# Optimization experiments

Measured on AMD Instinct MI355X. Metric: run time of the kernel, lower is better.

The kernel has to match this reference:

```python
import jax, jax.numpy as jnp
import numpy as np

H = 256          # hidden_channels
NP, NJ, NC = 8192, 8192, 4096  # person / job_posting / company node counts
EA, EW, EP = 262144, 131072, 131072  # edge counts per relation


def _gcn(x_src, W, b, edge_index, num_src, num_dst):
    """Bipartite GCNConv: h = x_src @ W; out[dst] = sum_e norm_e * h[src_e] + b,
    norm = deg_out(src)^-1/2 * deg_in(dst)^-1/2 (symmetric GCN normalization)."""
    h = x_src @ W                                # [num_src, H]
    row, col = edge_index[0], edge_index[1]
    ones = jnp.ones(row.shape[0], dtype=h.dtype)
    deg_src = jax.ops.segment_sum(ones, row, num_segments=num_src)
    deg_dst = jax.ops.segment_sum(ones, col, num_segments=num_dst)
    dis_src = jnp.where(deg_src > 0, jax.lax.rsqrt(jnp.maximum(deg_src, 1e-12)), 0.0)
    dis_dst = jnp.where(deg_dst > 0, jax.lax.rsqrt(jnp.maximum(deg_dst, 1e-12)), 0.0)
    norm = dis_src[row] * dis_dst[col]           # [E]
    out = jax.ops.segment_sum(h[row] * norm[:, None], col, num_segments=num_dst)
    return out + b


def setup_inputs() -> dict:
    key = jax.random.key(0)
    ks = jax.random.split(key, 12)
    s = 1.0 / np.sqrt(H)
    return {
        "x_person":  jax.random.normal(ks[0], (NP, H), jnp.float32),
        "x_job":     jax.random.normal(ks[1], (NJ, H), jnp.float32),
        "x_company": jax.random.normal(ks[2], (NC, H), jnp.float32),
        "ei_applied": jax.random.randint(ks[3], (2, EA), 0, 8192, jnp.int64 if jax.config.read('jax_enable_x64') else jnp.int32),
        "ei_worked":  jax.random.randint(ks[4], (2, EW), 0, 4096, jnp.int64 if jax.config.read('jax_enable_x64') else jnp.int32),
        "ei_posted":  jax.random.randint(ks[5], (2, EP), 0, 4096, jnp.int64 if jax.config.read('jax_enable_x64') else jnp.int32),
        "W_aj": jax.random.normal(ks[6], (H, H), jnp.float32) * s,
        "b_aj": jnp.zeros((H,), jnp.float32),
        "W_wa": jax.random.normal(ks[7], (H, H), jnp.float32) * s,
        "b_wa": jnp.zeros((H,), jnp.float32),
        "W_pb": jax.random.normal(ks[8], (H, H), jnp.float32) * s,
        "b_pb": jnp.zeros((H,), jnp.float32),
    }


def reference(x_person, x_job, x_company, ei_applied, ei_worked, ei_posted,
              W_aj, b_aj, W_wa, b_wa, W_pb, b_pb):
    Np, Nj, Nc = x_person.shape[0], x_job.shape[0], x_company.shape[0]
    # HeteroConv with aggr='sum': each dst type sums messages over its edge types
    job_emb = _gcn(x_person, W_aj, b_aj, ei_applied, Np, Nj)
    comp_emb = (_gcn(x_person, W_wa, b_wa, ei_worked, Np, Nc)
                + _gcn(x_job, W_pb, b_pb, ei_posted, Nj, Nc))  # computed but unused downstream
    del comp_emb
    person_emb = x_person  # 'person' is never a dst type; features pass through
    scores = jax.nn.sigmoid(person_emb @ job_emb.T)  # [Np, Nj]
    return scores
```

## Files before the change

### kernel.cpp

```cpp
#include <hip/hip_runtime.h>
#include <hip/hip_bf16.h>

#define HCH 256
#define NPN 8192
#define NJN 8192
#define EAE 262144
#define CAP 96

typedef _Float16 f16x8 __attribute__((ext_vector_type(8)));
typedef _Float16 f16x4 __attribute__((ext_vector_type(4)));
typedef float f32x4 __attribute__((ext_vector_type(4)));

typedef __attribute__((address_space(1))) void glb_void;
typedef __attribute__((address_space(3))) void lds_void;

#define WS_CUR   0
#define WS_DEG   32768
#define WS_CSR2  65536
#define WS_XH    3211264
#define WS_ZH    7405568
#define WS_GH    11599872
#define WS_WHT   15794176

__global__ void k_edgeconv(const int* __restrict__ row, const int* __restrict__ col,
                           int* __restrict__ deg_src, int* __restrict__ cur,
                           int* __restrict__ csr2, const float* __restrict__ W,
                           _Float16* __restrict__ WhT, const float* __restrict__ x,
                           _Float16* __restrict__ Xh) {
    int bid = blockIdx.x, t = threadIdx.x;
    if (bid < 1024) {
        int e = bid * 256 + t;
        int r = row[e], c = col[e];
        atomicAdd(&deg_src[r], 1);
        int p = atomicAdd(&cur[c], 1);
        if (p < CAP) csr2[c * CAP + p] = r;
    } else if (bid < 1280) {
        int idx = (bid - 1024) * 256 + t;
        int n = idx >> 8, k = idx & 255;
        WhT[idx] = (_Float16)W[k * HCH + n];
    } else {
        int i = ((bid - 1280) * 256 + t) * 4;
        float4 v = *(const float4*)(x + i);
        f16x4 h;
        h[0] = (_Float16)v.x; h[1] = (_Float16)v.y;
        h[2] = (_Float16)v.z; h[3] = (_Float16)v.w;
        *(f16x4*)(Xh + i) = h;
    }
}

__global__ __launch_bounds__(64)
void k_agg(const _Float16* __restrict__ Xh, const int* __restrict__ csr2,
           const int* __restrict__ cur, const int* __restrict__ deg_src,
           _Float16* __restrict__ Zh) {
    int j = blockIdx.x;
    int t = threadIdx.x;
    int degt = cur[j];
    int deg = degt > CAP ? CAP : degt;

    __shared__ int   sidx[CAP];
    __shared__ float sw[CAP];
    for (int b = t; b < deg; b += 64) {
        int s = csr2[j * CAP + b];
        sidx[b] = s;
        sw[b] = rsqrtf((float)deg_src[s]);
    }
    __syncthreads();

    float a0 = 0.f, a1 = 0.f, a2 = 0.f, a3 = 0.f;
    const _Float16* xb = Xh + t * 4;
    int e = 0;
    for (; e + 4 <= deg; e += 4) {
        int s0 = sidx[e], s1 = sidx[e + 1], s2 = sidx[e + 2], s3 = sidx[e + 3];
        float w0 = sw[e], w1 = sw[e + 1], w2 = sw[e + 2], w3 = sw[e + 3];
        f16x4 v0 = *(const f16x4*)(xb + (size_t)s0 * HCH);
        f16x4 v1 = *(const f16x4*)(xb + (size_t)s1 * HCH);
        f16x4 v2 = *(const f16x4*)(xb + (size_t)s2 * HCH);
        f16x4 v3 = *(const f16x4*)(xb + (size_t)s3 * HCH);
        a0 += w0 * (float)v0[0] + w1 * (float)v1[0] + w2 * (float)v2[0] + w3 * (float)v3[0];
        a1 += w0 * (float)v0[1] + w1 * (float)v1[1] + w2 * (float)v2[1] + w3 * (float)v3[1];
        a2 += w0 * (float)v0[2] + w1 * (float)v1[2] + w2 * (float)v2[2] + w3 * (float)v3[2];
        a3 += w0 * (float)v0[3] + w1 * (float)v1[3] + w2 * (float)v2[3] + w3 * (float)v3[3];
    }
    for (; e < deg; e++) {
        int s0 = sidx[e];
        float w0 = sw[e];
        f16x4 v0 = *(const f16x4*)(xb + (size_t)s0 * HCH);
        a0 += w0 * (float)v0[0]; a1 += w0 * (float)v0[1];
        a2 += w0 * (float)v0[2]; a3 += w0 * (float)v0[3];
    }
    f16x4 out;
    if (degt > 0) {
        float dd = rsqrtf((float)degt);
        out[0] = (_Float16)(a0 * dd); out[1] = (_Float16)(a1 * dd);
        out[2] = (_Float16)(a2 * dd); out[3] = (_Float16)(a3 * dd);
    } else {
        out[0] = out[1] = out[2] = out[3] = (_Float16)0.f;
    }
    *(f16x4*)(Zh + (size_t)j * HCH + t * 4) = out;
}

template <int TM, int TN>
__global__ __launch_bounds__(256, 2)
void k_gemm(const _Float16* __restrict__ A, const _Float16* __restrict__ Bt,
            const float* __restrict__ bias, _Float16* __restrict__ Cout, int Ncols) {
    constexpr int WM = TM / 2, WN = TN / 2;
    constexpr int MR = WM / 16, NR = WN / 16;
    constexpr int CHA = TM * 8 / 256;
    constexpr int CHB = TN * 8 / 256;
    constexpr int BOFF = TM * 128;

    __shared__ _Float16 sm[2][(TM + TN) * 64];

    int tid = threadIdx.x;
    int wid = tid >> 6, lane = tid & 63;

    int brow = blockIdx.y * TM;
    int bcol = blockIdx.x * TN;
    int wrow = (wid >> 1) * WM;
    int wcol = (wid & 1) * WN;

    f32x4 acc[MR][NR] = {};

    int lr = lane & 15;
    int kq = lane >> 4;

    auto stage = [&](int t, int b) {
        int k0 = t * 64;
#pragma unroll
        for (int i = 0; i < CHA; i++) {
            int wc0 = i * 256 + wid * 64;
            int c = wc0 + lane;
            int r = c >> 3, cc = c & 7;
            const char* ga = (const char*)A +
                (size_t)(brow + r) * (HCH * 2) + (size_t)(k0 + cc * 8) * 2;
            __builtin_amdgcn_global_load_lds(
                (glb_void*)ga, (lds_void*)((char*)sm[b] + wc0 * 16), 16, 0, 0);
        }
#pragma unroll
        for (int i = 0; i < CHB; i++) {
            int wc0 = i * 256 + wid * 64;
            int c = wc0 + lane;
            int r = c >> 3, cc = c & 7;
            const char* gb = (const char*)Bt +
                (size_t)(bcol + r) * (HCH * 2) + (size_t)(k0 + cc * 8) * 2;
            __builtin_amdgcn_global_load_lds(
                (glb_void*)gb, (lds_void*)((char*)sm[b] + BOFF + wc0 * 16), 16, 0, 0);
        }
    };

    stage(0, 0);
    __syncthreads();

    constexpr int NT = HCH / 64;
#pragma unroll
    for (int t = 0; t < NT; t++) {
        int cur = t & 1;
        if (t + 1 < NT) stage(t + 1, cur ^ 1);
        const char* base = (const char*)sm[cur];
#pragma unroll
        for (int kk = 0; kk < 64; kk += 32) {
            f16x8 af[MR], bfr[NR];
            int kbyte = (kk + kq * 8) * 2;
#pragma unroll
            for (int m = 0; m < MR; m++) {
                int r = wrow + m * 16 + lr;
                af[m] = *(const f16x8*)(base + r * 128 + kbyte);
            }
#pragma unroll
            for (int n = 0; n < NR; n++) {
                int r = wcol + n * 16 + lr;
                bfr[n] = *(const f16x8*)(base + BOFF + r * 128 + kbyte);
            }
#pragma unroll
            for (int m = 0; m < MR; m++)
#pragma unroll
                for (int n = 0; n < NR; n++)
                    acc[m][n] = __builtin_amdgcn_mfma_f32_16x16x32_f16(
                        af[m], bfr[n], acc[m][n], 0, 0, 0);
        }
        __syncthreads();
    }

    int rq = lane >> 4;
#pragma unroll
    for (int m = 0; m < MR; m++) {
#pragma unroll
        for (int n = 0; n < NR; n++) {
#pragma unroll
            for (int j = 0; j < 4; j++) {
                int gr = brow + wrow + m * 16 + rq * 4 + j;
                int gc = bcol + wcol + n * 16 + lr;
                float v = acc[m][n][j] + bias[gc];
                Cout[(size_t)gr * Ncols + gc] = (_Float16)v;
            }
        }
    }
}

#define G2_NW 32
__global__ __launch_bounds__(512, 1)
void k_gemm2(const _Float16* __restrict__ A, const _Float16* __restrict__ Bt,
             float* __restrict__ C) {
    __shared__ _Float16 smA[128 * HCH];
    __shared__ _Float16 smB[2][64 * HCH];
    __shared__ float    smC[128 * 64];

    int tid = threadIdx.x;
    int wid = tid >> 6, lane = tid & 63;
    int lr = lane & 15, kq = lane >> 4;

    int id = blockIdx.x;
    int xcd = id & 7, slot = id >> 3;
    int cg = xcd >> 1;
    int strip = slot + (xcd & 1) * 32;
    int brow = strip * 128;
    int bcol0 = cg * (64 * G2_NW);

    int wrow = (wid >> 1) * 32;
    int wcol = (wid & 1) * 32;

#pragma unroll
    for (int i = 0; i < 8; i++) {
        int wc0 = i * 512 + wid * 64;
        int c = wc0 + lane;
        int r = c >> 5, q = c & 31;
        int j = q ^ (r & 7);
        const char* ga = (const char*)(A + (size_t)(brow + r) * HCH + j * 8);
        __builtin_amdgcn_global_load_lds(
            (glb_void*)ga, (lds_void*)((char*)smA + wc0 * 16), 16, 0, 0);
    }
    auto stageB = [&](int t, int b) {
#pragma unroll
        for (int i = 0; i < 4; i++) {
            int wc0 = i * 512 + wid * 64;
            int c = wc0 + lane;
            int r = c >> 5, q = c & 31;
            int j = q ^ (r & 7);
            const char* gb = (const char*)(Bt +
                (size_t)(bcol0 + t * 64 + r) * HCH + j * 8);
            __builtin_amdgcn_global_load_lds(
                (glb_void*)gb, (lds_void*)((char*)smB[b] + wc0 * 16), 16, 0, 0);
        }
    };
    stageB(0, 0);
    __syncthreads();

    const char* sA = (const char*)smA;
    f16x8 areg[2][8];
#pragma unroll
    for (int m = 0; m < 2; m++) {
#pragma unroll
        for (int ks = 0; ks < 8; ks++) {
            int r = wrow + m * 16 + lr;
            int sb = ks * 4 + kq;
            areg[m][ks] = *(const f16x8*)(sA + r * 512 + ((sb ^ (r & 7)) << 4));
        }
    }

    for (int t = 0; t < G2_NW; t++) {
        int cb = t & 1;
        if (t + 1 < G2_NW) stageB(t + 1, cb ^ 1);
        __builtin_amdgcn_sched_barrier(0);
        const char* sB = (const char*)smB[cb];
        f32x4 acc[2][2] = {};
        __builtin_amdgcn_s_setprio(1);
#pragma unroll
        for (int ks = 0; ks < 8; ks++) {
            f16x8 bf2[2];
            int sb = ks * 4 + kq;
#pragma unroll
            for (int n = 0; n < 2; n++) {
                int r = wcol + n * 16 + lr;
                bf2[n] = *(const f16x8*)(sB + r * 512 + ((sb ^ (r & 7)) << 4));
            }
#pragma unroll
            for (int m = 0; m < 2; m++)
#pragma unroll
                for (int n = 0; n < 2; n++)
                    acc[m][n] = __builtin_amdgcn_mfma_f32_16x16x32_f16(
                        bf2[n], areg[m][ks], acc[m][n], 0, 0, 0);
        }
        __builtin_amdgcn_s_setprio(0);

#pragma unroll
        for (int m = 0; m < 2; m++) {
#pragma unroll
            for (int n = 0; n < 2; n++) {
                int row = wrow + m * 16 + lr;
                int ch = ((wcol + n * 16) >> 2) + kq;
                int sc = ch ^ (row & 7);
                *(f32x4*)(smC + row * 64 + sc * 4) = acc[m][n];
            }
        }

        int bcol = bcol0 + t * 64;
        int ch = (wcol >> 2) + (lane & 7);
#pragma unroll
        for (int p = 0; p < 4; p++) {
            int row = wrow + p * 8 + (lane >> 3);
            int sc = ch ^ (row & 7);
            f32x4 v = *(const f32x4*)(smC + row * 64 + sc * 4);
            f32x4 o;
#pragma unroll
            for (int j = 0; j < 4; j++) {
                float e = __expf(-v[j]);
                o[j] = __builtin_amdgcn_rcpf(1.f + e);
            }
            __builtin_nontemporal_store(
                o, (f32x4*)(C + (size_t)(brow + row) * NJN + bcol + ch * 4));
        }

        if (t + 1 < G2_NW) {
            __builtin_amdgcn_sched_barrier(0);
            asm volatile("s_waitcnt vmcnt(4)" ::: "memory");
            __builtin_amdgcn_s_barrier();
            __builtin_amdgcn_sched_barrier(0);
        }
    }
}

extern "C" void kernel_launch(void* const* d_in, const int* in_sizes, int n_in,
                              void* d_out, int out_size, void* d_ws, size_t ws_size,
                              hipStream_t stream) {
    const float* x_person = (const float*)d_in[0];
    const int*   ei_app   = (const int*)d_in[3];
    const float* W_aj     = (const float*)d_in[6];
    const float* b_aj     = (const float*)d_in[7];

    const int* erow = ei_app;
    const int* ecol = ei_app + EAE;

    char* w = (char*)d_ws;
    int*      cur     = (int*)(w + WS_CUR);
    int*      deg_src = (int*)(w + WS_DEG);
    int*      csr2    = (int*)(w + WS_CSR2);
    _Float16* Xh      = (_Float16*)(w + WS_XH);
    _Float16* Zh      = (_Float16*)(w + WS_ZH);
    _Float16* Gh      = (_Float16*)(w + WS_GH);
    _Float16* WhT     = (_Float16*)(w + WS_WHT);

    hipMemsetAsync(w, 0, 65536, stream);
    k_edgeconv<<<3328, 256, 0, stream>>>(erow, ecol, deg_src, cur, csr2,
                                         W_aj, WhT, x_person, Xh);
    k_agg<<<NJN, 64, 0, stream>>>(Xh, csr2, cur, deg_src, Zh);
    {
        dim3 grid(HCH / 128, NJN / 64);
        k_gemm<64, 128><<<grid, 256, 0, stream>>>(Zh, WhT, b_aj, Gh, HCH);
    }
    k_gemm2<<<256, 512, 0, stream>>>(Xh, Gh, (float*)d_out);
}
```

Before: 127.4 us.

## Fuse edge conversion, aggregation and small GEMM into one cooperative kernel

Merges the edge/degree build, the neighbour aggregation and the Z·W GEMM into a single cooperative kernel of 256 blocks × 512 threads, separated by grid-wide syncs. It removes two kernel launches and their inter-kernel gaps. In exchange, each phase now runs on a fixed small grid: the aggregation uses one wave per destination node over four passes, and the GEMM uses 64×128 tiles with 8 waves. Grid sync overhead and lower occupancy per phase may offset the launch savings.

```diff
diff --git a/kernel.cpp b/kernel.cpp
--- a/kernel.cpp
+++ b/kernel.cpp
@@ -1,5 +1,8 @@
 #include <hip/hip_runtime.h>
 #include <hip/hip_bf16.h>
+#include <hip/hip_cooperative_groups.h>
+
+namespace cg = cooperative_groups;
 
 #define HCH 256
 #define NPN 8192
@@ -22,176 +25,170 @@
 #define WS_GH    11599872
 #define WS_WHT   15794176
 
-__global__ void k_edgeconv(const int* __restrict__ row, const int* __restrict__ col,
-                           int* __restrict__ deg_src, int* __restrict__ cur,
-                           int* __restrict__ csr2, const float* __restrict__ W,
-                           _Float16* __restrict__ WhT, const float* __restrict__ x,
-                           _Float16* __restrict__ Xh) {
-    int bid = blockIdx.x, t = threadIdx.x;
-    if (bid < 1024) {
-        int e = bid * 256 + t;
-        int r = row[e], c = col[e];
-        atomicAdd(&deg_src[r], 1);
-        int p = atomicAdd(&cur[c], 1);
-        if (p < CAP) csr2[c * CAP + p] = r;
-    } else if (bid < 1280) {
-        int idx = (bid - 1024) * 256 + t;
-        int n = idx >> 8, k = idx & 255;
-        WhT[idx] = (_Float16)W[k * HCH + n];
-    } else {
-        int i = ((bid - 1280) * 256 + t) * 4;
-        float4 v = *(const float4*)(x + i);
-        f16x4 h;
-        h[0] = (_Float16)v.x; h[1] = (_Float16)v.y;
-        h[2] = (_Float16)v.z; h[3] = (_Float16)v.w;
-        *(f16x4*)(Xh + i) = h;
-    }
-}
-
-__global__ __launch_bounds__(64)
-void k_agg(const _Float16* __restrict__ Xh, const int* __restrict__ csr2,
-           const int* __restrict__ cur, const int* __restrict__ deg_src,
-           _Float16* __restrict__ Zh) {
-    int j = blockIdx.x;
-    int t = threadIdx.x;
-    int degt = cur[j];
-    int deg = degt > CAP ? CAP : degt;
-
-    __shared__ int   sidx[CAP];
-    __shared__ float sw[CAP];
-    for (int b = t; b < deg; b += 64) {
-        int s = csr2[j * CAP + b];
-        sidx[b] = s;
-        sw[b] = rsqrtf((float)deg_src[s]);
-    }
-    __syncthreads();
-
-    float a0 = 0.f, a1 = 0.f, a2 = 0.f, a3 = 0.f;
-    const _Float16* xb = Xh + t * 4;
-    int e = 0;
-    for (; e + 4 <= deg; e += 4) {
-        int s0 = sidx[e], s1 = sidx[e + 1], s2 = sidx[e + 2], s3 = sidx[e + 3];
-        float w0 = sw[e], w1 = sw[e + 1], w2 = sw[e + 2], w3 = sw[e + 3];
-        f16x4 v0 = *(const f16x4*)(xb + (size_t)s0 * HCH);
-        f16x4 v1 = *(const f16x4*)(xb + (size_t)s1 * HCH);
-        f16x4 v2 = *(const f16x4*)(xb + (size_t)s2 * HCH);
-        f16x4 v3 = *(const f16x4*)(xb + (size_t)s3 * HCH);
-        a0 += w0 * (float)v0[0] + w1 * (float)v1[0] + w2 * (float)v2[0] + w3 * (float)v3[0];
-        a1 += w0 * (float)v0[1] + w1 * (float)v1[1] + w2 * (float)v2[1] + w3 * (float)v3[1];
-        a2 += w0 * (float)v0[2] + w1 * (float)v1[2] + w2 * (float)v2[2] + w3 * (float)v3[2];
-        a3 += w0 * (float)v0[3] + w1 * (float)v1[3] + w2 * (float)v2[3] + w3 * (float)v3[3];
-    }
-    for (; e < deg; e++) {
-        int s0 = sidx[e];
-        float w0 = sw[e];
-        f16x4 v0 = *(const f16x4*)(xb + (size_t)s0 * HCH);
-        a0 += w0 * (float)v0[0]; a1 += w0 * (float)v0[1];
-        a2 += w0 * (float)v0[2]; a3 += w0 * (float)v0[3];
-    }
-    f16x4 out;
-    if (degt > 0) {
-        float dd = rsqrtf((float)degt);
-        out[0] = (_Float16)(a0 * dd); out[1] = (_Float16)(a1 * dd);
-        out[2] = (_Float16)(a2 * dd); out[3] = (_Float16)(a3 * dd);
-    } else {
-        out[0] = out[1] = out[2] = out[3] = (_Float16)0.f;
-    }
-    *(f16x4*)(Zh + (size_t)j * HCH + t * 4) = out;
-}
-
-template <int TM, int TN>
-__global__ __launch_bounds__(256, 2)
-void k_gemm(const _Float16* __restrict__ A, const _Float16* __restrict__ Bt,
-            const float* __restrict__ bias, _Float16* __restrict__ Cout, int Ncols) {
-    constexpr int WM = TM / 2, WN = TN / 2;
-    constexpr int MR = WM / 16, NR = WN / 16;
-    constexpr int CHA = TM * 8 / 256;
-    constexpr int CHB = TN * 8 / 256;
-    constexpr int BOFF = TM * 128;
-
-    __shared__ _Float16 sm[2][(TM + TN) * 64];
-
+__global__ void k_fused(const int* __restrict__ row, const int* __restrict__ col,
+                        int* __restrict__ deg_src, int* __restrict__ cur,
+                        int* __restrict__ csr2, const float* __restrict__ W,
+                        _Float16* __restrict__ WhT, const float* __restrict__ x,
+                        _Float16* __restrict__ Xh, _Float16* __restrict__ Zh,
+                        const float* __restrict__ bias, _Float16* __restrict__ Gh) {
+    __shared__ __align__(16) char ubuf[49152];
+
+    int bid = blockIdx.x;
     int tid = threadIdx.x;
     int wid = tid >> 6, lane = tid & 63;
-
-    int brow = blockIdx.y * TM;
-    int bcol = blockIdx.x * TN;
-    int wrow = (wid >> 1) * WM;
-    int wcol = (wid & 1) * WN;
-
-    f32x4 acc[MR][NR] = {};
-
-    int lr = lane & 15;
-    int kq = lane >> 4;
-
-    auto stage = [&](int t, int b) {
-        int k0 = t * 64;
-#pragma unroll
-        for (int i = 0; i < CHA; i++) {
-            int wc0 = i * 256 + wid * 64;
-            int c = wc0 + lane;
-            int r = c >> 3, cc = c & 7;
-            const char* ga = (const char*)A +
-                (size_t)(brow + r) * (HCH * 2) + (size_t)(k0 + cc * 8) * 2;
-            __builtin_amdgcn_global_load_lds(
-                (glb_void*)ga, (lds_void*)((char*)sm[b] + wc0 * 16), 16, 0, 0);
-        }
-#pragma unroll
-        for (int i = 0; i < CHB; i++) {
-            int wc0 = i * 256 + wid * 64;
-            int c = wc0 + lane;
-            int r = c >> 3, cc = c & 7;
-            const char* gb = (const char*)Bt +
-                (size_t)(bcol + r) * (HCH * 2) + (size_t)(k0 + cc * 8) * 2;
-            __builtin_amdgcn_global_load_lds(
-                (glb_void*)gb, (lds_void*)((char*)sm[b] + BOFF + wc0 * 16), 16, 0, 0);
-        }
-    };
-
-    stage(0, 0);
-    __syncthreads();
-
-    constexpr int NT = HCH / 64;
-#pragma unroll
-    for (int t = 0; t < NT; t++) {
-        int cur = t & 1;
-        if (t + 1 < NT) stage(t + 1, cur ^ 1);
-        const char* base = (const char*)sm[cur];
-#pragma unroll
-        for (int kk = 0; kk < 64; kk += 32) {
-            f16x8 af[MR], bfr[NR];
-            int kbyte = (kk + kq * 8) * 2;
-#pragma unroll
-            for (int m = 0; m < MR; m++) {
-                int r = wrow + m * 16 + lr;
-                af[m] = *(const f16x8*)(base + r * 128 + kbyte);
-            }
-#pragma unroll
-            for (int n = 0; n < NR; n++) {
-                int r = wcol + n * 16 + lr;
-                bfr[n] = *(const f16x8*)(base + BOFF + r * 128 + kbyte);
-            }
-#pragma unroll
-            for (int m = 0; m < MR; m++)
-#pragma unroll
-                for (int n = 0; n < NR; n++)
-                    acc[m][n] = __builtin_amdgcn_mfma_f32_16x16x32_f16(
-                        af[m], bfr[n], acc[m][n], 0, 0, 0);
-        }
+    int lr = lane & 15, kq = lane >> 4;
+    cg::grid_group grid = cg::this_grid();
+
+    {
+        int g = bid * 512 + tid;
+#pragma unroll
+        for (int it = 0; it < 2; it++) {
+            int e = g + it * 131072;
+            int r = row[e], c = col[e];
+            atomicAdd(&deg_src[r], 1);
+            int p = atomicAdd(&cur[c], 1);
+            if (p < CAP) csr2[c * CAP + p] = r;
+        }
+        if (g < 65536) {
+            int n = g >> 8, k = g & 255;
+            WhT[g] = (_Float16)W[k * HCH + n];
+        }
+#pragma unroll
+        for (int it = 0; it < 4; it++) {
+            int i = (g + it * 131072) * 4;
+            float4 v = *(const float4*)(x + i);
+            f16x4 h;
+            h[0] = (_Float16)v.x; h[1] = (_Float16)v.y;
+            h[2] = (_Float16)v.z; h[3] = (_Float16)v.w;
+            *(f16x4*)(Xh + i) = h;
+        }
+    }
+    grid.sync();
+
+    {
+        int* sidx = (int*)(ubuf + wid * 768);
+        float* sw = (float*)(ubuf + wid * 768 + 384);
+        int wgid = bid * 8 + wid;
+#pragma unroll
+        for (int pass = 0; pass < 4; pass++) {
+            int j = wgid + pass * 2048;
+            int degt = cur[j];
+            int deg = degt > CAP ? CAP : degt;
+            for (int b = lane; b < deg; b += 64) {
+                int s = csr2[j * CAP + b];
+                sidx[b] = s;
+                sw[b] = rsqrtf((float)deg_src[s]);
+            }
+            float a0 = 0.f, a1 = 0.f, a2 = 0.f, a3 = 0.f;
+            const _Float16* xb = Xh + lane * 4;
+            int e = 0;
+            for (; e + 4 <= deg; e += 4) {
+                int s0 = sidx[e], s1 = sidx[e + 1], s2 = sidx[e + 2], s3 = sidx[e + 3];
+                float w0 = sw[e], w1 = sw[e + 1], w2 = sw[e + 2], w3 = sw[e + 3];
+                f16x4 v0 = *(const f16x4*)(xb + (size_t)s0 * HCH);
+                f16x4 v1 = *(const f16x4*)(xb + (size_t)s1 * HCH);
+                f16x4 v2 = *(const f16x4*)(xb + (size_t)s2 * HCH);
+                f16x4 v3 = *(const f16x4*)(xb + (size_t)s3 * HCH);
+                a0 += w0 * (float)v0[0] + w1 * (float)v1[0] + w2 * (float)v2[0] + w3 * (float)v3[0];
+                a1 += w0 * (float)v0[1] + w1 * (float)v1[1] + w2 * (float)v2[1] + w3 * (float)v3[1];
+                a2 += w0 * (float)v0[2] + w1 * (float)v1[2] + w2 * (float)v2[2] + w3 * (float)v3[2];
+                a3 += w0 * (float)v0[3] + w1 * (float)v1[3] + w2 * (float)v2[3] + w3 * (float)v3[3];
+            }
+            for (; e < deg; e++) {
+                int s0 = sidx[e];
+                float w0 = sw[e];
+                f16x4 v0 = *(const f16x4*)(xb + (size_t)s0 * HCH);
+                a0 += w0 * (float)v0[0]; a1 += w0 * (float)v0[1];
+                a2 += w0 * (float)v0[2]; a3 += w0 * (float)v0[3];
+            }
+            f16x4 out;
+            if (degt > 0) {
+                float dd = rsqrtf((float)degt);
+                out[0] = (_Float16)(a0 * dd); out[1] = (_Float16)(a1 * dd);
+                out[2] = (_Float16)(a2 * dd); out[3] = (_Float16)(a3 * dd);
+            } else {
+                out[0] = out[1] = out[2] = out[3] = (_Float16)0.f;
+            }
+            *(f16x4*)(Zh + (size_t)j * HCH + lane * 4) = out;
+        }
+    }
+    grid.sync();
+
+    {
+        int bx = bid & 1, by = bid >> 1;
+        int brow = by * 64, bcol = bx * 128;
+        int wrow = (wid >> 2) * 32;
+        int wcol = (wid & 3) * 32;
+        constexpr int BUFB = 24576;
+        constexpr int BOFF = 8192;
+
+        auto stage = [&](int t, int b) {
+            int k0 = t * 64;
+            char* base = ubuf + b * BUFB;
+            {
+                int wc0 = wid * 64;
+                int c = wc0 + lane;
+                int r = c >> 3, cc = c & 7;
+                const char* ga = (const char*)(Zh + (size_t)(brow + r) * HCH + k0 + cc * 8);
+                __builtin_amdgcn_global_load_lds(
+                    (glb_void*)ga, (lds_void*)(base + wc0 * 16), 16, 0, 0);
+            }
+#pragma unroll
+            for (int i = 0; i < 2; i++) {
+                int wc0 = i * 512 + wid * 64;
+                int c = wc0 + lane;
+                int r = c >> 3, cc = c & 7;
+                const char* gb = (const char*)(WhT + (size_t)(bcol + r) * HCH + k0 + cc * 8);
+                __builtin_amdgcn_global_load_lds(
+                    (glb_void*)gb, (lds_void*)(base + BOFF + wc0 * 16), 16, 0, 0);
+            }
+        };
+
+        f32x4 acc[2][2] = {};
+        stage(0, 0);
         __syncthreads();
-    }
-
-    int rq = lane >> 4;
-#pragma unroll
-    for (int m = 0; m < MR; m++) {
-#pragma unroll
-        for (int n = 0; n < NR; n++) {
-#pragma unroll
-            for (int j = 0; j < 4; j++) {
-                int gr = brow + wrow + m * 16 + rq * 4 + j;
-                int gc = bcol + wcol + n * 16 + lr;
-                float v = acc[m][n][j] + bias[gc];
-                Cout[(size_t)gr * Ncols + gc] = (_Float16)v;
+
+#pragma unroll
+        for (int t = 0; t < 4; t++) {
+            int cb = t & 1;
+            if (t + 1 < 4) stage(t + 1, cb ^ 1);
+            const char* base = ubuf + cb * BUFB;
+#pragma unroll
+            for (int kk = 0; kk < 64; kk += 32) {
+                f16x8 af[2], bfr[2];
+                int kbyte = (kk + kq * 8) * 2;
+#pragma unroll
+                for (int m = 0; m < 2; m++) {
+                    int r = wrow + m * 16 + lr;
+                    af[m] = *(const f16x8*)(base + r * 128 + kbyte);
+                }
+#pragma unroll
+                for (int n = 0; n < 2; n++) {
+                    int r = wcol + n * 16 + lr;
+                    bfr[n] = *(const f16x8*)(base + BOFF + r * 128 + kbyte);
+                }
+#pragma unroll
+                for (int m = 0; m < 2; m++)
+#pragma unroll
+                    for (int n = 0; n < 2; n++)
+                        acc[m][n] = __builtin_amdgcn_mfma_f32_16x16x32_f16(
+                            af[m], bfr[n], acc[m][n], 0, 0, 0);
+            }
+            __syncthreads();
+        }
+
+        int rq = lane >> 4;
+#pragma unroll
+        for (int m = 0; m < 2; m++) {
+#pragma unroll
+            for (int n = 0; n < 2; n++) {
+#pragma unroll
+                for (int j = 0; j < 4; j++) {
+                    int gr = brow + wrow + m * 16 + rq * 4 + j;
+                    int gc = bcol + wcol + n * 16 + lr;
+                    float v = acc[m][n][j] + bias[gc];
+                    Gh[(size_t)gr * HCH + gc] = (_Float16)v;
+                }
             }
         }
     }
@@ -211,10 +208,10 @@
 
     int id = blockIdx.x;
     int xcd = id & 7, slot = id >> 3;
-    int cg = xcd >> 1;
+    int cg2 = xcd >> 1;
     int strip = slot + (xcd & 1) * 32;
     int brow = strip * 128;
-    int bcol0 = cg * (64 * G2_NW);
+    int bcol0 = cg2 * (64 * G2_NW);
 
     int wrow = (wid >> 1) * 32;
     int wcol = (wid & 1) * 32;
@@ -340,12 +337,12 @@
     _Float16* WhT     = (_Float16*)(w + WS_WHT);
 
     hipMemsetAsync(w, 0, 65536, stream);
-    k_edgeconv<<<3328, 256, 0, stream>>>(erow, ecol, deg_src, cur, csr2,
-                                         W_aj, WhT, x_person, Xh);
-    k_agg<<<NJN, 64, 0, stream>>>(Xh, csr2, cur, deg_src, Zh);
     {
-        dim3 grid(HCH / 128, NJN / 64);
-        k_gemm<64, 128><<<grid, 256, 0, stream>>>(Zh, WhT, b_aj, Gh, HCH);
+        void* kargs[] = {(void*)&erow, (void*)&ecol, (void*)&deg_src, (void*)&cur,
+                         (void*)&csr2, (void*)&W_aj, (void*)&WhT, (void*)&x_person,
+                         (void*)&Xh, (void*)&Zh, (void*)&b_aj, (void*)&Gh};
+        hipLaunchCooperativeKernel((void*)k_fused, dim3(256), dim3(512),
+                                   kargs, 0, stream);
     }
     k_gemm2<<<256, 512, 0, stream>>>(Xh, Gh, (float*)d_out);
 }
```

New measurement: 208.6 us. +63.8%, slower.
